# Performance work log

Hardware: AMD Instinct MI355X
Metric: run time of the kernel (lower is better)

Reference implementation:

```python
import jax, jax.numpy as jnp
import numpy as np
import math

B, N, C = 8, 2048, 512

def setup_inputs() -> dict:
    key = jax.random.key(0)
    ks = jax.random.split(key, 7)
    s = 1.0 / math.sqrt(C)
    return {
        "feature": jax.random.normal(ks[0], (B, N, C), dtype=jnp.float32),
        "wq": jax.random.uniform(ks[1], (C, C), jnp.float32, -s, s),
        "bq": jax.random.uniform(ks[2], (C,), jnp.float32, -s, s),
        "wk": jax.random.uniform(ks[3], (C, C), jnp.float32, -s, s),
        "bk": jax.random.uniform(ks[4], (C,), jnp.float32, -s, s),
        "wv": jax.random.uniform(ks[5], (C, C), jnp.float32, -s, s),
        "bv": jax.random.uniform(ks[6], (C,), jnp.float32, -s, s),
    }

def reference(feature, wq, bq, wk, bk, wv, bv):
    # torch nn.Linear: x @ W.T + b
    q = jnp.einsum('bnc,dc->bnd', feature, wq) + bq
    k = jnp.einsum('bnc,dc->bnd', feature, wk) + bk
    v = jnp.einsum('bnc,dc->bnd', feature, wv) + bv
    scores = jnp.einsum('bnd,bmd->bnm', q, k)          # [B, N, N]
    attn = jax.nn.softmax(scores, axis=2) / math.sqrt(C)  # post-softmax scale (as in source)
    v_star = jnp.einsum('bnm,bmd->bnd', attn, v)
    return feature + v_star
```

## Files before the change

### kernel.cpp

```cpp
#include <hip/hip_runtime.h>
#include <cstdint>
#include <cstddef>


typedef __bf16 bf16x8 __attribute__((ext_vector_type(8)));
typedef float f32x4 __attribute__((ext_vector_type(4)));
typedef short short4v __attribute__((ext_vector_type(4)));

__device__ __forceinline__ short f2b(float f) {
  union { float f; unsigned u; } u; u.f = f;
  unsigned r = (u.u + 0x7fffu + ((u.u >> 16) & 1u)) >> 16;
  return (short)r;
}

#define GLDS(gptr, lptr) \
  __builtin_amdgcn_global_load_lds( \
      (const __attribute__((address_space(1))) unsigned int*)(const void*)(gptr), \
      (__attribute__((address_space(3))) unsigned int*)(void*)(lptr), 16, 0, 0)

__device__ __forceinline__ bf16x8 ldfrag64(const short* buf, int row, int kq) {
  return *(const bf16x8*)(buf + row * 64 + ((kq ^ (row & 7)) * 8));
}

__device__ __forceinline__ bf16x8 ldfrag32(const short* buf, int row, int l4) {
  const short* p = buf + row * 32 + ((l4 ^ ((row >> 1) & 3)) * 8);
  bf16x8 r;
  asm volatile("ds_read_b128 %0, %1"
               : "=v"(r)
               : "v"((const __attribute__((address_space(3))) short*)(const void*)p));
  return r;
}

#define LGKM0_SB() do { \
    asm volatile("s_waitcnt lgkmcnt(0)" ::: "memory"); \
    __builtin_amdgcn_sched_barrier(0); } while (0)
#define VMW(n) asm volatile("s_waitcnt vmcnt(" #n ")" ::: "memory")
#define SBAR() __builtin_amdgcn_s_barrier()
#define PRIO1() __builtin_amdgcn_s_setprio(1)
#define PRIO0() __builtin_amdgcn_s_setprio(0)

__global__ __launch_bounds__(256) void prep(const float* __restrict__ f,
                                            const float* __restrict__ w0,
                                            const float* __restrict__ w1,
                                            const float* __restrict__ w2,
                                            const float* __restrict__ b0,
                                            const float* __restrict__ b1,
                                            const float* __restrict__ b2,
                                            short* __restrict__ Xb, short* __restrict__ Wb,
                                            float* __restrict__ biasP, float* __restrict__ l) {
  const int bid = blockIdx.x;
  const int t = threadIdx.x;
  if (bid < 8192) {
    int i = bid * 256 + t;
    float4 v = ((const float4*)f)[i];
    short4v o = { f2b(v.x), f2b(v.y), f2b(v.z), f2b(v.w) };
    *(short4v*)(Xb + (size_t)i * 4) = o;
  } else if (bid < 8960) {
    int i = (bid - 8192) * 256 + t;
    const float* src = (i < 65536) ? w0 : (i < 131072) ? w1 : w2;
    float4 v = ((const float4*)src)[i & 65535];
    short4v o = { f2b(v.x), f2b(v.y), f2b(v.z), f2b(v.w) };
    *(short4v*)(Wb + (size_t)i * 4) = o;
  } else {
    int i = (bid - 8960) * 256 + t;
    float4 z = { 0.f, 0.f, 0.f, 0.f };
    ((float4*)l)[i * 2] = z;
    ((float4*)l)[i * 2 + 1] = z;
    if (i < 1536) {
      const float* s = (i < 512) ? b0 : (i < 1024) ? b1 : b2;
      biasP[i] = s[i & 511];
    }
  }
}

__global__ __launch_bounds__(256) void gemm_qkv(const short* __restrict__ X,
                                                const short* __restrict__ Wall,
                                                const float* __restrict__ biasP,
                                                short* __restrict__ Out,
                                                short* __restrict__ VtOut) {
  __shared__ __align__(16) short Xs[128 * 64];
  __shared__ __align__(16) short Ws[128 * 64];
  const int z = blockIdx.z;
  const short* Wm = Wall + (size_t)z * 262144;
  const int m0 = blockIdx.y * 128, n0 = blockIdx.x * 128;
  const int t = threadIdx.x;
  const int lane = t & 63, w = t >> 6;
  const int wn = (w & 1) * 64, wm = (w >> 1) * 64;
  const int fr = lane & 15, l4 = lane >> 4;

  f32x4 acc[4][4] = {};

  for (int k0 = 0; k0 < 512; k0 += 64) {
    __syncthreads();
#pragma unroll
    for (int u = 0; u < 4; ++u) {
      int cc = t + u * 256;
      int r = cc >> 3, cs = cc & 7;
      int kk = ((cs ^ (r & 7)) * 8);
      GLDS(X + (size_t)(m0 + r) * 512 + k0 + kk, Xs + cc * 8);
      GLDS(Wm + (size_t)(n0 + r) * 512 + k0 + kk, Ws + cc * 8);
    }
    __syncthreads();
#pragma unroll
    for (int h = 0; h < 2; ++h) {
      bf16x8 wf[4], xf[4];
#pragma unroll
      for (int i = 0; i < 4; ++i) wf[i] = ldfrag64(Ws, wn + i * 16 + fr, h * 4 + l4);
#pragma unroll
      for (int j = 0; j < 4; ++j) xf[j] = ldfrag64(Xs, wm + j * 16 + fr, h * 4 + l4);
      if (z < 2) {
#pragma unroll
        for (int i = 0; i < 4; ++i)
#pragma unroll
          for (int j = 0; j < 4; ++j)
            acc[i][j] = __builtin_amdgcn_mfma_f32_16x16x32_bf16(wf[i], xf[j], acc[i][j], 0, 0, 0);
      } else {
#pragma unroll
        for (int i = 0; i < 4; ++i)
#pragma unroll
          for (int j = 0; j < 4; ++j)
            acc[i][j] = __builtin_amdgcn_mfma_f32_16x16x32_bf16(xf[i], wf[j], acc[i][j], 0, 0, 0);
      }
    }
  }

  const int rq = l4 * 4;
  if (z < 2) {
#pragma unroll
    for (int i = 0; i < 4; ++i) {
      int nb = n0 + wn + i * 16 + rq;
      float4 bs = *(const float4*)(biasP + z * 512 + nb);
#pragma unroll
      for (int j = 0; j < 4; ++j) {
        int m = m0 + wm + j * 16 + fr;
        short4v o = { f2b(acc[i][j][0] + bs.x), f2b(acc[i][j][1] + bs.y),
                      f2b(acc[i][j][2] + bs.z), f2b(acc[i][j][3] + bs.w) };
        *(short4v*)(Out + (size_t)z * 8388608 + (size_t)m * 512 + nb) = o;
      }
    }
  } else {
    const int zB = blockIdx.y >> 4;
    const int mb = m0 & 2047;
#pragma unroll
    for (int j = 0; j < 4; ++j) {
      int d = n0 + wn + j * 16 + fr;
      float bd = biasP[1024 + d];
#pragma unroll
      for (int i = 0; i < 4; ++i) {
        int mloc = mb + wm + i * 16 + rq;
        short4v o = { f2b(acc[i][j][0] + bd), f2b(acc[i][j][1] + bd),
                      f2b(acc[i][j][2] + bd), f2b(acc[i][j][3] + bd) };
        *(short4v*)(VtOut + (size_t)zB * 1048576 + (size_t)d * 2048 + mloc) = o;
      }
    }
  }
}

__global__ __launch_bounds__(256) void gemm_qk8(const short* __restrict__ Q,
                                                const short* __restrict__ Kb,
                                                short* __restrict__ P,
                                                float* __restrict__ l) {
  __shared__ __align__(16) short As[2][4096];
  __shared__ __align__(16) short Bs[2][4096];
  const int id = blockIdx.x + blockIdx.y * 16 + blockIdx.z * 256;
  const int swz = (id & 7) * 256 + (id >> 3);
  const int z = swz >> 8;
  const int m0 = (swz & 15) * 128;
  const int n0 = ((swz >> 4) & 15) * 128;
  const short* __restrict__ A = Kb + (size_t)z * 1048576;
  const short* __restrict__ B = Q + (size_t)z * 1048576;
  const int t = threadIdx.x;
  const int lane = t & 63, w = t >> 6;
  const int aw = (w >> 1) * 64, bw = (w & 1) * 64;
  const int fr = lane & 15, l4 = lane >> 4;
  const int r0 = t >> 2, cs = t & 3;
  const int csw = (cs ^ ((r0 >> 1) & 3)) * 8;
  const short* pA = A + (size_t)(m0 + r0) * 512 + csw;
  const short* pB = B + (size_t)(n0 + r0) * 512 + csw;

#define QK_STG(buf, kt) do { \
    GLDS(pA + (kt) * 32, &As[(buf)][t * 8]); \
    GLDS(pA + 64 * 512 + (kt) * 32, &As[(buf)][2048 + t * 8]); \
    GLDS(pB + (kt) * 32, &Bs[(buf)][t * 8]); \
    GLDS(pB + 64 * 512 + (kt) * 32, &Bs[(buf)][2048 + t * 8]); \
  } while (0)

  f32x4 acc[4][4] = {};
  bf16x8 a[4], b[4];

  QK_STG(0, 0); QK_STG(1, 1);

#pragma unroll 1
  for (int kt = 0; kt < 16; ++kt) {
    const int c = kt & 1;
    if (kt >= 1 && kt < 15) QK_STG(c ^ 1, kt + 1);
    if (kt < 15) { VMW(4); } else { VMW(0); }
    SBAR();
#pragma unroll
    for (int i = 0; i < 4; ++i) a[i] = ldfrag32(&As[c][0], aw + i * 16 + fr, l4);
#pragma unroll
    for (int n = 0; n < 4; ++n) b[n] = ldfrag32(&Bs[c][0], bw + n * 16 + fr, l4);
    LGKM0_SB(); PRIO1();
#pragma unroll
    for (int i = 0; i < 4; ++i)
#pragma unroll
      for (int n = 0; n < 4; ++n)
        acc[i][n] = __builtin_amdgcn_mfma_f32_16x16x32_bf16(a[i], b[n], acc[i][n], 0, 0, 0);
    PRIO0(); SBAR();
  }
#undef QK_STG

  const float LOG2E = 1.4426950408889634f;
  float rs[4] = { 0.f, 0.f, 0.f, 0.f };
#pragma unroll
  for (int i = 0; i < 4; ++i) {
    const int key = m0 + aw + i * 16 + l4 * 4;
#pragma unroll
    for (int n = 0; n < 4; ++n) {
      const int q = n0 + bw + n * 16 + fr;
      short4v o;
      float part = 0.f;
#pragma unroll
      for (int r = 0; r < 4; ++r) {
        float e = exp2f(acc[i][n][r] * LOG2E);
        o[r] = f2b(e);
        part += e;
      }
      *(short4v*)(P + (size_t)z * 4194304 + (size_t)q * 2048 + key) = o;
      rs[n] += part;
    }
  }
#pragma unroll
  for (int n = 0; n < 4; ++n) {
    rs[n] += __shfl_xor(rs[n], 16);
    rs[n] += __shfl_xor(rs[n], 32);
  }
  if (l4 == 0) {
#pragma unroll
    for (int n = 0; n < 4; ++n)
      atomicAdd(&l[z * 2048 + n0 + bw + n * 16 + fr], rs[n]);
  }
}

__global__ __launch_bounds__(256) void gemm_pv8(const short* __restrict__ Pm,
                                                const short* __restrict__ Vt,
                                                const float* __restrict__ l,
                                                const float* __restrict__ resid,
                                                float* __restrict__ out, float scale) {
  __shared__ __align__(16) short As[2][4096];
  __shared__ __align__(16) short Bs[2][4096];
  const int id = blockIdx.x + blockIdx.y * 4 + blockIdx.z * 64;
  const int swz = (id & 7) * 64 + (id >> 3);
  const int z = swz >> 6;
  const int d0 = (swz & 3) * 128;
  const int n0 = ((swz >> 2) & 15) * 128;
  const short* __restrict__ A = Vt + (size_t)z * 1048576;
  const short* __restrict__ B = Pm + (size_t)z * 4194304;
  const int t = threadIdx.x;
  const int lane = t & 63, w = t >> 6;
  const int aw = (w >> 1) * 64, bw = (w & 1) * 64;
  const int fr = lane & 15, l4 = lane >> 4;
  const int r0 = t >> 2, cs = t & 3;
  const int csw = (cs ^ ((r0 >> 1) & 3)) * 8;
  const short* pA = A + (size_t)(d0 + r0) * 2048 + csw;
  const short* pB = B + (size_t)(n0 + r0) * 2048 + csw;

#define PV_STG(buf, kt) do { \
    GLDS(pA + (kt) * 32, &As[(buf)][t * 8]); \
    GLDS(pA + (size_t)64 * 2048 + (kt) * 32, &As[(buf)][2048 + t * 8]); \
    GLDS(pB + (kt) * 32, &Bs[(buf)][t * 8]); \
    GLDS(pB + (size_t)64 * 2048 + (kt) * 32, &Bs[(buf)][2048 + t * 8]); \
  } while (0)

  f32x4 acc[4][4] = {};
  bf16x8 a[4], b[4];

  PV_STG(0, 0); PV_STG(1, 1);

#pragma unroll 1
  for (int kt = 0; kt < 64; ++kt) {
    const int c = kt & 1;
    if (kt >= 1 && kt < 63) PV_STG(c ^ 1, kt + 1);
    if (kt < 63) { VMW(4); } else { VMW(0); }
    SBAR();
#pragma unroll
    for (int i = 0; i < 4; ++i) a[i] = ldfrag32(&As[c][0], aw + i * 16 + fr, l4);
#pragma unroll
    for (int n = 0; n < 4; ++n) b[n] = ldfrag32(&Bs[c][0], bw + n * 16 + fr, l4);
    LGKM0_SB(); PRIO1();
#pragma unroll
    for (int i = 0; i < 4; ++i)
#pragma unroll
      for (int n = 0; n < 4; ++n)
        acc[i][n] = __builtin_amdgcn_mfma_f32_16x16x32_bf16(a[i], b[n], acc[i][n], 0, 0, 0);
    PRIO0(); SBAR();
  }
#undef PV_STG

  float linv[4];
#pragma unroll
  for (int n = 0; n < 4; ++n) {
    const int q = n0 + bw + n * 16 + fr;
    linv[n] = scale / l[z * 2048 + q];
  }
#pragma unroll
  for (int n = 0; n < 4; ++n) {
    const int q = n0 + bw + n * 16 + fr;
#pragma unroll
    for (int i = 0; i < 4; ++i) {
      const int d = d0 + aw + i * 16 + l4 * 4;
      const size_t idx = (size_t)z * 1048576 + (size_t)q * 512 + d;
      float4 rv = *(const float4*)(resid + idx);
      float4 o = { rv.x + acc[i][n][0] * linv[n], rv.y + acc[i][n][1] * linv[n],
                   rv.z + acc[i][n][2] * linv[n], rv.w + acc[i][n][3] * linv[n] };
      *(float4*)(out + idx) = o;
    }
  }
}

extern "C" void kernel_launch(void* const* d_in, const int* in_sizes, int n_in,
                              void* d_out, int out_size, void* d_ws, size_t ws_size,
                              hipStream_t stream) {
  const float* feature = (const float*)d_in[0];
  const float* wq = (const float*)d_in[1];
  const float* bq = (const float*)d_in[2];
  const float* wk = (const float*)d_in[3];
  const float* bk = (const float*)d_in[4];
  const float* wv = (const float*)d_in[5];
  const float* bv = (const float*)d_in[6];
  float* out = (float*)d_out;

  const size_t MN = (size_t)16384 * 512;
  short* Xb = (short*)d_ws;
  short* Wb = Xb + MN;
  short* Q = Wb + 786432;
  short* K = Q + MN;
  short* Vt = K + MN;
  short* P = Vt + MN;
  float* biasP = (float*)(P + (size_t)8 * 2048 * 2048);
  float* l = biasP + 1536;

  prep<<<8968, 256, 0, stream>>>(feature, wq, wk, wv, bq, bk, bv, Xb, Wb, biasP, l);

  gemm_qkv<<<dim3(4, 128, 3), 256, 0, stream>>>(Xb, Wb, biasP, Q, Vt);
  gemm_qk8<<<dim3(16, 16, 8), 256, 0, stream>>>(Q, K, P, l);

  const float iscl = 0.044194173824159216f;
  gemm_pv8<<<dim3(4, 16, 8), 256, 0, stream>>>(P, Vt, l, feature, out, iscl);
}
```

Baseline: 238.3 us.

## Restructure QK and PV GEMMs with resident K tile and register-streamed V

The QK kernel now keeps a full 128x512 K tile resident in LDS per block and loops over four 256-query tiles, streaming only Q through double-buffered LDS. This cuts repeated K loads and moves to 512-thread blocks on a 256-block grid. The PV kernel gives each block 64 queries across all 512 output dims. P is streamed through a triple-buffered LDS ring, and V^T fragments are loaded straight from global into registers with one-step prefetch. The larger LDS footprint and register use, plus a grid of only 256 blocks, lower occupancy and may leave CUs underused.

```diff
diff --git a/kernel.cpp b/kernel.cpp
--- a/kernel.cpp
+++ b/kernel.cpp
@@ -22,13 +22,21 @@
   return *(const bf16x8*)(buf + row * 64 + ((kq ^ (row & 7)) * 8));
 }
 
-__device__ __forceinline__ bf16x8 ldfrag32(const short* buf, int row, int l4) {
-  const short* p = buf + row * 32 + ((l4 ^ ((row >> 1) & 3)) * 8);
+__device__ __forceinline__ bf16x8 ds_asm(const short* p) {
   bf16x8 r;
   asm volatile("ds_read_b128 %0, %1"
                : "=v"(r)
                : "v"((const __attribute__((address_space(3))) short*)(const void*)p));
   return r;
+}
+__device__ __forceinline__ bf16x8 ldfragA(const short* buf, int row, int c) {
+  return ds_asm(buf + row * 512 + ((c ^ (row & 7)) * 8));
+}
+__device__ __forceinline__ bf16x8 ldfrag32(const short* buf, int row, int l4) {
+  return ds_asm(buf + row * 32 + ((l4 ^ ((row >> 1) & 3)) * 8));
+}
+__device__ __forceinline__ bf16x8 ldfragP(const short* buf, int row, int c) {
+  return ds_asm(buf + row * 64 + ((c ^ (row & 7)) * 8));
 }
 
 #define LGKM0_SB() do { \
@@ -156,159 +164,193 @@
   }
 }
 
-__global__ __launch_bounds__(256) void gemm_qk8(const short* __restrict__ Q,
+__global__ __launch_bounds__(512) void gemm_qk9(const short* __restrict__ Q,
                                                 const short* __restrict__ Kb,
                                                 short* __restrict__ P,
                                                 float* __restrict__ l) {
-  __shared__ __align__(16) short As[2][4096];
-  __shared__ __align__(16) short Bs[2][4096];
-  const int id = blockIdx.x + blockIdx.y * 16 + blockIdx.z * 256;
-  const int swz = (id & 7) * 256 + (id >> 3);
-  const int z = swz >> 8;
-  const int m0 = (swz & 15) * 128;
-  const int n0 = ((swz >> 4) & 15) * 128;
-  const short* __restrict__ A = Kb + (size_t)z * 1048576;
-  const short* __restrict__ B = Q + (size_t)z * 1048576;
+  __shared__ __align__(16) short As[128 * 512];
+  __shared__ __align__(16) short Bs[2][256 * 32];
+  const int id = blockIdx.x;
+  const int z = id & 7;
+  const int kb = (id >> 3) & 15;
+  const int qh = id >> 7;
+  const int m0 = kb * 128;
+  const short* __restrict__ Ag = Kb + (size_t)z * 1048576 + (size_t)m0 * 512;
+  const short* __restrict__ Bg = Q + (size_t)z * 1048576 + (size_t)(qh * 1024) * 512;
   const int t = threadIdx.x;
   const int lane = t & 63, w = t >> 6;
-  const int aw = (w >> 1) * 64, bw = (w & 1) * 64;
+  const int aw = (w >> 2) * 64, bw = (w & 3) * 64;
   const int fr = lane & 15, l4 = lane >> 4;
-  const int r0 = t >> 2, cs = t & 3;
-  const int csw = (cs ^ ((r0 >> 1) & 3)) * 8;
-  const short* pA = A + (size_t)(m0 + r0) * 512 + csw;
-  const short* pB = B + (size_t)(n0 + r0) * 512 + csw;
-
-#define QK_STG(buf, kt) do { \
-    GLDS(pA + (kt) * 32, &As[(buf)][t * 8]); \
-    GLDS(pA + 64 * 512 + (kt) * 32, &As[(buf)][2048 + t * 8]); \
-    GLDS(pB + (kt) * 32, &Bs[(buf)][t * 8]); \
-    GLDS(pB + 64 * 512 + (kt) * 32, &Bs[(buf)][2048 + t * 8]); \
+  const int br = t >> 2, bc = t & 3;
+  const int bcs1 = (bc ^ ((br >> 1) & 3)) * 8;
+  const int bcs2 = (bc ^ (((br + 128) >> 1) & 3)) * 8;
+
+#define QK_STG_B(buf, qt, kt) do { \
+    GLDS(Bg + (size_t)((qt) * 256 + br) * 512 + (kt) * 32 + bcs1, &Bs[(buf)][t * 8]); \
+    GLDS(Bg + (size_t)((qt) * 256 + br + 128) * 512 + (kt) * 32 + bcs2, \
+         &Bs[(buf)][4096 + t * 8]); \
   } while (0)
 
+#pragma unroll
+  for (int j = 0; j < 16; ++j) {
+    int Lc = t + j * 512;
+    int r = Lc >> 6, c = Lc & 63;
+    GLDS(Ag + (size_t)r * 512 + (c ^ (r & 7)) * 8, As + Lc * 8);
+  }
+  QK_STG_B(0, 0, 0);
+  VMW(0);
+  SBAR();
+
   f32x4 acc[4][4] = {};
-  bf16x8 a[4], b[4];
-
-  QK_STG(0, 0); QK_STG(1, 1);
-
+  const float LOG2E = 1.4426950408889634f;
+
+  for (int qt = 0; qt < 4; ++qt) {
 #pragma unroll 1
-  for (int kt = 0; kt < 16; ++kt) {
-    const int c = kt & 1;
-    if (kt >= 1 && kt < 15) QK_STG(c ^ 1, kt + 1);
-    if (kt < 15) { VMW(4); } else { VMW(0); }
-    SBAR();
-#pragma unroll
-    for (int i = 0; i < 4; ++i) a[i] = ldfrag32(&As[c][0], aw + i * 16 + fr, l4);
-#pragma unroll
-    for (int n = 0; n < 4; ++n) b[n] = ldfrag32(&Bs[c][0], bw + n * 16 + fr, l4);
-    LGKM0_SB(); PRIO1();
-#pragma unroll
-    for (int i = 0; i < 4; ++i)
+    for (int kt = 0; kt < 16; ++kt) {
+      const int p = qt * 16 + kt;
+      const int c = kt & 1;
+      if (p < 63) {
+        const int pn = p + 1;
+        QK_STG_B(c ^ 1, pn >> 4, pn & 15);
+        VMW(2);
+      } else {
+        VMW(0);
+      }
+      SBAR();
+      bf16x8 af[4], bf[4];
+#pragma unroll
+      for (int i = 0; i < 4; ++i) af[i] = ldfragA(As, aw + i * 16 + fr, kt * 4 + l4);
+#pragma unroll
+      for (int n = 0; n < 4; ++n) bf[n] = ldfrag32(&Bs[c][0], bw + n * 16 + fr, l4);
+      LGKM0_SB(); PRIO1();
+#pragma unroll
+      for (int i = 0; i < 4; ++i)
+#pragma unroll
+        for (int n = 0; n < 4; ++n)
+          acc[i][n] = __builtin_amdgcn_mfma_f32_16x16x32_bf16(af[i], bf[n], acc[i][n], 0, 0, 0);
+      PRIO0(); SBAR();
+    }
+    const int qbase = qh * 1024 + qt * 256;
+    float rs[4] = { 0.f, 0.f, 0.f, 0.f };
+#pragma unroll
+    for (int i = 0; i < 4; ++i) {
+      const int key = m0 + aw + i * 16 + l4 * 4;
+#pragma unroll
+      for (int n = 0; n < 4; ++n) {
+        const int q = qbase + bw + n * 16 + fr;
+        short4v o;
+        float part = 0.f;
+#pragma unroll
+        for (int r = 0; r < 4; ++r) {
+          float e = exp2f(acc[i][n][r] * LOG2E);
+          o[r] = f2b(e);
+          part += e;
+        }
+        *(short4v*)(P + (size_t)z * 4194304 + (size_t)q * 2048 + key) = o;
+        rs[n] += part;
+        acc[i][n] = (f32x4){ 0.f, 0.f, 0.f, 0.f };
+      }
+    }
+#pragma unroll
+    for (int n = 0; n < 4; ++n) {
+      rs[n] += __shfl_xor(rs[n], 16);
+      rs[n] += __shfl_xor(rs[n], 32);
+    }
+    if (l4 == 0) {
 #pragma unroll
       for (int n = 0; n < 4; ++n)
-        acc[i][n] = __builtin_amdgcn_mfma_f32_16x16x32_bf16(a[i], b[n], acc[i][n], 0, 0, 0);
-    PRIO0(); SBAR();
-  }
-#undef QK_STG
-
-  const float LOG2E = 1.4426950408889634f;
-  float rs[4] = { 0.f, 0.f, 0.f, 0.f };
-#pragma unroll
-  for (int i = 0; i < 4; ++i) {
-    const int key = m0 + aw + i * 16 + l4 * 4;
-#pragma unroll
-    for (int n = 0; n < 4; ++n) {
-      const int q = n0 + bw + n * 16 + fr;
-      short4v o;
-      float part = 0.f;
-#pragma unroll
-      for (int r = 0; r < 4; ++r) {
-        float e = exp2f(acc[i][n][r] * LOG2E);
-        o[r] = f2b(e);
-        part += e;
-      }
-      *(short4v*)(P + (size_t)z * 4194304 + (size_t)q * 2048 + key) = o;
-      rs[n] += part;
-    }
-  }
-#pragma unroll
-  for (int n = 0; n < 4; ++n) {
-    rs[n] += __shfl_xor(rs[n], 16);
-    rs[n] += __shfl_xor(rs[n], 32);
-  }
-  if (l4 == 0) {
-#pragma unroll
-    for (int n = 0; n < 4; ++n)
-      atomicAdd(&l[z * 2048 + n0 + bw + n * 16 + fr], rs[n]);
-  }
-}
-
-__global__ __launch_bounds__(256) void gemm_pv8(const short* __restrict__ Pm,
+        atomicAdd(&l[z * 2048 + qbase + bw + n * 16 + fr], rs[n]);
+    }
+  }
+#undef QK_STG_B
+}
+
+__global__ __launch_bounds__(512) void gemm_pv9(const short* __restrict__ Pm,
                                                 const short* __restrict__ Vt,
                                                 const float* __restrict__ l,
                                                 const float* __restrict__ resid,
                                                 float* __restrict__ out, float scale) {
-  __shared__ __align__(16) short As[2][4096];
-  __shared__ __align__(16) short Bs[2][4096];
-  const int id = blockIdx.x + blockIdx.y * 4 + blockIdx.z * 64;
-  const int swz = (id & 7) * 64 + (id >> 3);
-  const int z = swz >> 6;
-  const int d0 = (swz & 3) * 128;
-  const int n0 = ((swz >> 2) & 15) * 128;
-  const short* __restrict__ A = Vt + (size_t)z * 1048576;
-  const short* __restrict__ B = Pm + (size_t)z * 4194304;
+  __shared__ __align__(16) short Ps[3][64 * 64];
+  const int id = blockIdx.x;
+  const int z = id & 7;
+  const int q0 = (id >> 3) * 64;
+  const short* __restrict__ Pg = Pm + (size_t)z * 4194304 + (size_t)q0 * 2048;
+  const short* __restrict__ Vg = Vt + (size_t)z * 1048576;
   const int t = threadIdx.x;
   const int lane = t & 63, w = t >> 6;
-  const int aw = (w >> 1) * 64, bw = (w & 1) * 64;
+  const int dw = w * 64;
   const int fr = lane & 15, l4 = lane >> 4;
-  const int r0 = t >> 2, cs = t & 3;
-  const int csw = (cs ^ ((r0 >> 1) & 3)) * 8;
-  const short* pA = A + (size_t)(d0 + r0) * 2048 + csw;
-  const short* pB = B + (size_t)(n0 + r0) * 2048 + csw;
-
-#define PV_STG(buf, kt) do { \
-    GLDS(pA + (kt) * 32, &As[(buf)][t * 8]); \
-    GLDS(pA + (size_t)64 * 2048 + (kt) * 32, &As[(buf)][2048 + t * 8]); \
-    GLDS(pB + (kt) * 32, &Bs[(buf)][t * 8]); \
-    GLDS(pB + (size_t)64 * 2048 + (kt) * 32, &Bs[(buf)][2048 + t * 8]); \
-  } while (0)
+  const int pr = t >> 3, pc = t & 7;
+  const int pcs = (pc ^ (pr & 7)) * 8;
+
+#define PV_STG_P(s, kt) GLDS(Pg + (size_t)pr * 2048 + (kt) * 64 + pcs, &Ps[(s)][t * 8])
+
+  const short* vbase = Vg + (size_t)(dw + fr) * 2048 + l4 * 8;
 
   f32x4 acc[4][4] = {};
-  bf16x8 a[4], b[4];
-
-  PV_STG(0, 0); PV_STG(1, 1);
+  bf16x8 vc[4][2], vn[4][2];
+
+  PV_STG_P(0, 0);
+  PV_STG_P(1, 1);
+#pragma unroll
+  for (int i = 0; i < 4; ++i)
+#pragma unroll
+    for (int kk = 0; kk < 2; ++kk)
+      vc[i][kk] = *(const bf16x8*)(vbase + (size_t)i * 16 * 2048 + kk * 32);
+  VMW(0);
+  SBAR();
 
 #pragma unroll 1
-  for (int kt = 0; kt < 64; ++kt) {
-    const int c = kt & 1;
-    if (kt >= 1 && kt < 63) PV_STG(c ^ 1, kt + 1);
-    if (kt < 63) { VMW(4); } else { VMW(0); }
+  for (int kt = 0; kt < 32; ++kt) {
+    if (kt < 31) {
+#pragma unroll
+      for (int i = 0; i < 4; ++i)
+#pragma unroll
+        for (int kk = 0; kk < 2; ++kk)
+          vn[i][kk] = *(const bf16x8*)(vbase + (size_t)i * 16 * 2048 +
+                                       (size_t)(kt + 1) * 64 + kk * 32);
+    }
+    if (kt < 30) PV_STG_P((kt + 2) % 3, kt + 2);
+    bf16x8 pf[4][2];
+    {
+      const short* Pc = &Ps[kt % 3][0];
+#pragma unroll
+      for (int n = 0; n < 4; ++n)
+#pragma unroll
+        for (int kk = 0; kk < 2; ++kk)
+          pf[n][kk] = ldfragP(Pc, n * 16 + fr, kk * 4 + l4);
+    }
+    if (kt < 30) { VMW(9); } else if (kt == 30) { VMW(8); } else { VMW(0); }
     SBAR();
-#pragma unroll
-    for (int i = 0; i < 4; ++i) a[i] = ldfrag32(&As[c][0], aw + i * 16 + fr, l4);
-#pragma unroll
-    for (int n = 0; n < 4; ++n) b[n] = ldfrag32(&Bs[c][0], bw + n * 16 + fr, l4);
     LGKM0_SB(); PRIO1();
 #pragma unroll
-    for (int i = 0; i < 4; ++i)
-#pragma unroll
-      for (int n = 0; n < 4; ++n)
-        acc[i][n] = __builtin_amdgcn_mfma_f32_16x16x32_bf16(a[i], b[n], acc[i][n], 0, 0, 0);
+    for (int kk = 0; kk < 2; ++kk)
+#pragma unroll
+      for (int i = 0; i < 4; ++i)
+#pragma unroll
+        for (int n = 0; n < 4; ++n)
+          acc[i][n] = __builtin_amdgcn_mfma_f32_16x16x32_bf16(vc[i][kk], pf[n][kk],
+                                                              acc[i][n], 0, 0, 0);
     PRIO0(); SBAR();
-  }
-#undef PV_STG
+    if (kt < 31) {
+#pragma unroll
+      for (int i = 0; i < 4; ++i)
+#pragma unroll
+        for (int kk = 0; kk < 2; ++kk) vc[i][kk] = vn[i][kk];
+    }
+  }
+#undef PV_STG_P
 
   float linv[4];
 #pragma unroll
+  for (int n = 0; n < 4; ++n)
+    linv[n] = scale / l[z * 2048 + q0 + n * 16 + fr];
+#pragma unroll
   for (int n = 0; n < 4; ++n) {
-    const int q = n0 + bw + n * 16 + fr;
-    linv[n] = scale / l[z * 2048 + q];
-  }
-#pragma unroll
-  for (int n = 0; n < 4; ++n) {
-    const int q = n0 + bw + n * 16 + fr;
+    const int q = q0 + n * 16 + fr;
 #pragma unroll
     for (int i = 0; i < 4; ++i) {
-      const int d = d0 + aw + i * 16 + l4 * 4;
+      const int d = dw + i * 16 + l4 * 4;
       const size_t idx = (size_t)z * 1048576 + (size_t)q * 512 + d;
       float4 rv = *(const float4*)(resid + idx);
       float4 o = { rv.x + acc[i][n][0] * linv[n], rv.y + acc[i][n][1] * linv[n],
@@ -343,8 +385,8 @@
   prep<<<8968, 256, 0, stream>>>(feature, wq, wk, wv, bq, bk, bv, Xb, Wb, biasP, l);
 
   gemm_qkv<<<dim3(4, 128, 3), 256, 0, stream>>>(Xb, Wb, biasP, Q, Vt);
-  gemm_qk8<<<dim3(16, 16, 8), 256, 0, stream>>>(Q, K, P, l);
+  gemm_qk9<<<256, 512, 0, stream>>>(Q, K, P, l);
 
   const float iscl = 0.044194173824159216f;
-  gemm_pv8<<<dim3(4, 16, 8), 256, 0, stream>>>(P, Vt, l, feature, out, iscl);
-}
+  gemm_pv9<<<256, 512, 0, stream>>>(P, Vt, l, feature, out, iscl);
+}
```

Result: slower. 287.5 us (+20.7%).

## Enlarge QK and PV GEMM tiles to 1024-thread blocks with K=64 stages

Applied to the files above, without the earlier changes.

Both attention GEMMs move from 128x128 tiles with 256 threads to 1024-thread blocks: QK uses 256x256 tiles and PV uses 128x256 tiles, each with a K step of 64 and an 8-way XOR swizzle. The pipeline changes from prefetching two stages ahead to issuing the next stage's global-to-LDS load after the fragment reads, with a full vmcnt(0) wait per iteration. The larger tiles are meant to cut global and L2 traffic through more reuse, at the cost of far fewer blocks (512 and 256), higher LDS use per block, and a shallower prefetch that may expose memory latency.

```diff
diff --git a/kernel.cpp b/kernel.cpp
--- a/kernel.cpp
+++ b/kernel.cpp
@@ -22,19 +22,21 @@
   return *(const bf16x8*)(buf + row * 64 + ((kq ^ (row & 7)) * 8));
 }
 
-__device__ __forceinline__ bf16x8 ldfrag32(const short* buf, int row, int l4) {
-  const short* p = buf + row * 32 + ((l4 ^ ((row >> 1) & 3)) * 8);
+__device__ __forceinline__ bf16x8 ds_asm(const short* p) {
   bf16x8 r;
   asm volatile("ds_read_b128 %0, %1"
                : "=v"(r)
                : "v"((const __attribute__((address_space(3))) short*)(const void*)p));
   return r;
 }
+__device__ __forceinline__ bf16x8 ldfrag64a(const short* buf, int row, int kq) {
+  return ds_asm(buf + row * 64 + ((kq ^ (row & 7)) * 8));
+}
 
 #define LGKM0_SB() do { \
     asm volatile("s_waitcnt lgkmcnt(0)" ::: "memory"); \
     __builtin_amdgcn_sched_barrier(0); } while (0)
-#define VMW(n) asm volatile("s_waitcnt vmcnt(" #n ")" ::: "memory")
+#define VMW0() asm volatile("s_waitcnt vmcnt(0)" ::: "memory")
 #define SBAR() __builtin_amdgcn_s_barrier()
 #define PRIO1() __builtin_amdgcn_s_setprio(1)
 #define PRIO0() __builtin_amdgcn_s_setprio(0)
@@ -156,57 +158,70 @@
   }
 }
 
-__global__ __launch_bounds__(256) void gemm_qk8(const short* __restrict__ Q,
-                                                const short* __restrict__ Kb,
-                                                short* __restrict__ P,
-                                                float* __restrict__ l) {
-  __shared__ __align__(16) short As[2][4096];
-  __shared__ __align__(16) short Bs[2][4096];
-  const int id = blockIdx.x + blockIdx.y * 16 + blockIdx.z * 256;
-  const int swz = (id & 7) * 256 + (id >> 3);
-  const int z = swz >> 8;
-  const int m0 = (swz & 15) * 128;
-  const int n0 = ((swz >> 4) & 15) * 128;
-  const short* __restrict__ A = Kb + (size_t)z * 1048576;
-  const short* __restrict__ B = Q + (size_t)z * 1048576;
+__global__ __launch_bounds__(1024) void gemm_qk10(const short* __restrict__ Q,
+                                                  const short* __restrict__ Kb,
+                                                  short* __restrict__ P,
+                                                  float* __restrict__ l) {
+  __shared__ __align__(16) short As[2][16384];
+  __shared__ __align__(16) short Bs[2][16384];
+  const int id = blockIdx.x;
+  const int z = id & 7, r = id >> 3;
+  const int m0 = (r & 7) * 256;
+  const int n0 = (r >> 3) * 256;
+  const short* __restrict__ A = Kb + (size_t)z * 1048576 + (size_t)m0 * 512;
+  const short* __restrict__ B = Q + (size_t)z * 1048576 + (size_t)n0 * 512;
   const int t = threadIdx.x;
   const int lane = t & 63, w = t >> 6;
-  const int aw = (w >> 1) * 64, bw = (w & 1) * 64;
+  const int aw = (w >> 2) * 64, bw = (w & 3) * 64;
   const int fr = lane & 15, l4 = lane >> 4;
-  const int r0 = t >> 2, cs = t & 3;
-  const int csw = (cs ^ ((r0 >> 1) & 3)) * 8;
-  const short* pA = A + (size_t)(m0 + r0) * 512 + csw;
-  const short* pB = B + (size_t)(n0 + r0) * 512 + csw;
+  const int sr = t >> 3, sc = t & 7;
+  const int swz = (sc ^ (sr & 7)) * 8;
+  const short* pA = A + (size_t)sr * 512 + swz;
+  const short* pB = B + (size_t)sr * 512 + swz;
 
 #define QK_STG(buf, kt) do { \
-    GLDS(pA + (kt) * 32, &As[(buf)][t * 8]); \
-    GLDS(pA + 64 * 512 + (kt) * 32, &As[(buf)][2048 + t * 8]); \
-    GLDS(pB + (kt) * 32, &Bs[(buf)][t * 8]); \
-    GLDS(pB + 64 * 512 + (kt) * 32, &Bs[(buf)][2048 + t * 8]); \
+    GLDS(pA + (kt) * 64, &As[(buf)][t * 8]); \
+    GLDS(pA + (size_t)128 * 512 + (kt) * 64, &As[(buf)][(t + 1024) * 8]); \
+    GLDS(pB + (kt) * 64, &Bs[(buf)][t * 8]); \
+    GLDS(pB + (size_t)128 * 512 + (kt) * 64, &Bs[(buf)][(t + 1024) * 8]); \
   } while (0)
 
   f32x4 acc[4][4] = {};
   bf16x8 a[4], b[4];
 
-  QK_STG(0, 0); QK_STG(1, 1);
-
-#pragma unroll 1
-  for (int kt = 0; kt < 16; ++kt) {
+  QK_STG(0, 0);
+  VMW0();
+  SBAR();
+
+#pragma unroll 2
+  for (int kt = 0; kt < 8; ++kt) {
     const int c = kt & 1;
-    if (kt >= 1 && kt < 15) QK_STG(c ^ 1, kt + 1);
-    if (kt < 15) { VMW(4); } else { VMW(0); }
+#pragma unroll
+    for (int i = 0; i < 4; ++i) a[i] = ldfrag64a(&As[c][0], aw + i * 16 + fr, l4);
+#pragma unroll
+    for (int n = 0; n < 4; ++n) b[n] = ldfrag64a(&Bs[c][0], bw + n * 16 + fr, l4);
+    if (kt < 7) QK_STG(c ^ 1, kt + 1);
     SBAR();
-#pragma unroll
-    for (int i = 0; i < 4; ++i) a[i] = ldfrag32(&As[c][0], aw + i * 16 + fr, l4);
-#pragma unroll
-    for (int n = 0; n < 4; ++n) b[n] = ldfrag32(&Bs[c][0], bw + n * 16 + fr, l4);
-    LGKM0_SB(); PRIO1();
+    LGKM0_SB();
+    PRIO1();
 #pragma unroll
     for (int i = 0; i < 4; ++i)
 #pragma unroll
       for (int n = 0; n < 4; ++n)
         acc[i][n] = __builtin_amdgcn_mfma_f32_16x16x32_bf16(a[i], b[n], acc[i][n], 0, 0, 0);
-    PRIO0(); SBAR();
+#pragma unroll
+    for (int i = 0; i < 4; ++i) a[i] = ldfrag64a(&As[c][0], aw + i * 16 + fr, 4 + l4);
+#pragma unroll
+    for (int n = 0; n < 4; ++n) b[n] = ldfrag64a(&Bs[c][0], bw + n * 16 + fr, 4 + l4);
+    LGKM0_SB();
+#pragma unroll
+    for (int i = 0; i < 4; ++i)
+#pragma unroll
+      for (int n = 0; n < 4; ++n)
+        acc[i][n] = __builtin_amdgcn_mfma_f32_16x16x32_bf16(a[i], b[n], acc[i][n], 0, 0, 0);
+    PRIO0();
+    if (kt < 7) VMW0();
+    SBAR();
   }
 #undef QK_STG
 
@@ -221,9 +236,9 @@
       short4v o;
       float part = 0.f;
 #pragma unroll
-      for (int r = 0; r < 4; ++r) {
-        float e = exp2f(acc[i][n][r] * LOG2E);
-        o[r] = f2b(e);
+      for (int rr = 0; rr < 4; ++rr) {
+        float e = exp2f(acc[i][n][rr] * LOG2E);
+        o[rr] = f2b(e);
         part += e;
       }
       *(short4v*)(P + (size_t)z * 4194304 + (size_t)q * 2048 + key) = o;
@@ -242,70 +257,80 @@
   }
 }
 
-__global__ __launch_bounds__(256) void gemm_pv8(const short* __restrict__ Pm,
-                                                const short* __restrict__ Vt,
-                                                const float* __restrict__ l,
-                                                const float* __restrict__ resid,
-                                                float* __restrict__ out, float scale) {
-  __shared__ __align__(16) short As[2][4096];
-  __shared__ __align__(16) short Bs[2][4096];
-  const int id = blockIdx.x + blockIdx.y * 4 + blockIdx.z * 64;
-  const int swz = (id & 7) * 64 + (id >> 3);
-  const int z = swz >> 6;
-  const int d0 = (swz & 3) * 128;
-  const int n0 = ((swz >> 2) & 15) * 128;
-  const short* __restrict__ A = Vt + (size_t)z * 1048576;
-  const short* __restrict__ B = Pm + (size_t)z * 4194304;
+__global__ __launch_bounds__(1024) void gemm_pv10(const short* __restrict__ Pm,
+                                                  const short* __restrict__ Vt,
+                                                  const float* __restrict__ l,
+                                                  const float* __restrict__ resid,
+                                                  float* __restrict__ out, float scale) {
+  __shared__ __align__(16) short As[2][8192];
+  __shared__ __align__(16) short Bs[2][16384];
+  const int id = blockIdx.x;
+  const int z = id & 7, r = id >> 3;
+  const int d0 = (r & 3) * 128;
+  const int q0 = (r >> 2) * 256;
+  const short* __restrict__ A = Vt + (size_t)z * 1048576 + (size_t)d0 * 2048;
+  const short* __restrict__ B = Pm + (size_t)z * 4194304 + (size_t)q0 * 2048;
   const int t = threadIdx.x;
   const int lane = t & 63, w = t >> 6;
-  const int aw = (w >> 1) * 64, bw = (w & 1) * 64;
+  const int aw = (w >> 3) * 64, bw = (w & 7) * 32;
   const int fr = lane & 15, l4 = lane >> 4;
-  const int r0 = t >> 2, cs = t & 3;
-  const int csw = (cs ^ ((r0 >> 1) & 3)) * 8;
-  const short* pA = A + (size_t)(d0 + r0) * 2048 + csw;
-  const short* pB = B + (size_t)(n0 + r0) * 2048 + csw;
+  const int sr = t >> 3, sc = t & 7;
+  const int swz = (sc ^ (sr & 7)) * 8;
+  const short* pA = A + (size_t)sr * 2048 + swz;
+  const short* pB = B + (size_t)sr * 2048 + swz;
 
 #define PV_STG(buf, kt) do { \
-    GLDS(pA + (kt) * 32, &As[(buf)][t * 8]); \
-    GLDS(pA + (size_t)64 * 2048 + (kt) * 32, &As[(buf)][2048 + t * 8]); \
-    GLDS(pB + (kt) * 32, &Bs[(buf)][t * 8]); \
-    GLDS(pB + (size_t)64 * 2048 + (kt) * 32, &Bs[(buf)][2048 + t * 8]); \
+    GLDS(pA + (kt) * 64, &As[(buf)][t * 8]); \
+    GLDS(pB + (kt) * 64, &Bs[(buf)][t * 8]); \
+    GLDS(pB + (size_t)128 * 2048 + (kt) * 64, &Bs[(buf)][(t + 1024) * 8]); \
   } while (0)
 
-  f32x4 acc[4][4] = {};
-  bf16x8 a[4], b[4];
-
-  PV_STG(0, 0); PV_STG(1, 1);
-
-#pragma unroll 1
-  for (int kt = 0; kt < 64; ++kt) {
+  f32x4 acc[4][2] = {};
+  bf16x8 a[4], b[2];
+
+  PV_STG(0, 0);
+  VMW0();
+  SBAR();
+
+#pragma unroll 2
+  for (int kt = 0; kt < 32; ++kt) {
     const int c = kt & 1;
-    if (kt >= 1 && kt < 63) PV_STG(c ^ 1, kt + 1);
-    if (kt < 63) { VMW(4); } else { VMW(0); }
+#pragma unroll
+    for (int i = 0; i < 4; ++i) a[i] = ldfrag64a(&As[c][0], aw + i * 16 + fr, l4);
+#pragma unroll
+    for (int n = 0; n < 2; ++n) b[n] = ldfrag64a(&Bs[c][0], bw + n * 16 + fr, l4);
+    if (kt < 31) PV_STG(c ^ 1, kt + 1);
     SBAR();
-#pragma unroll
-    for (int i = 0; i < 4; ++i) a[i] = ldfrag32(&As[c][0], aw + i * 16 + fr, l4);
-#pragma unroll
-    for (int n = 0; n < 4; ++n) b[n] = ldfrag32(&Bs[c][0], bw + n * 16 + fr, l4);
-    LGKM0_SB(); PRIO1();
+    LGKM0_SB();
+    PRIO1();
 #pragma unroll
     for (int i = 0; i < 4; ++i)
 #pragma unroll
-      for (int n = 0; n < 4; ++n)
+      for (int n = 0; n < 2; ++n)
         acc[i][n] = __builtin_amdgcn_mfma_f32_16x16x32_bf16(a[i], b[n], acc[i][n], 0, 0, 0);
-    PRIO0(); SBAR();
+#pragma unroll
+    for (int i = 0; i < 4; ++i) a[i] = ldfrag64a(&As[c][0], aw + i * 16 + fr, 4 + l4);
+#pragma unroll
+    for (int n = 0; n < 2; ++n) b[n] = ldfrag64a(&Bs[c][0], bw + n * 16 + fr, 4 + l4);
+    LGKM0_SB();
+#pragma unroll
+    for (int i = 0; i < 4; ++i)
+#pragma unroll
+      for (int n = 0; n < 2; ++n)
+        acc[i][n] = __builtin_amdgcn_mfma_f32_16x16x32_bf16(a[i], b[n], acc[i][n], 0, 0, 0);
+    PRIO0();
+    if (kt < 31) VMW0();
+    SBAR();
   }
 #undef PV_STG
 
-  float linv[4];
-#pragma unroll
-  for (int n = 0; n < 4; ++n) {
-    const int q = n0 + bw + n * 16 + fr;
-    linv[n] = scale / l[z * 2048 + q];
-  }
-#pragma unroll
-  for (int n = 0; n < 4; ++n) {
-    const int q = n0 + bw + n * 16 + fr;
+  float linv[2];
+#pragma unroll
+  for (int n = 0; n < 2; ++n)
+    linv[n] = scale / l[z * 2048 + q0 + bw + n * 16 + fr];
+#pragma unroll
+  for (int n = 0; n < 2; ++n) {
+    const int q = q0 + bw + n * 16 + fr;
 #pragma unroll
     for (int i = 0; i < 4; ++i) {
       const int d = d0 + aw + i * 16 + l4 * 4;
@@ -343,8 +368,8 @@
   prep<<<8968, 256, 0, stream>>>(feature, wq, wk, wv, bq, bk, bv, Xb, Wb, biasP, l);
 
   gemm_qkv<<<dim3(4, 128, 3), 256, 0, stream>>>(Xb, Wb, biasP, Q, Vt);
-  gemm_qk8<<<dim3(16, 16, 8), 256, 0, stream>>>(Q, K, P, l);
+  gemm_qk10<<<512, 1024, 0, stream>>>(Q, K, P, l);
 
   const float iscl = 0.044194173824159216f;
-  gemm_pv8<<<dim3(4, 16, 8), 256, 0, stream>>>(P, Vt, l, feature, out, iscl);
-}
+  gemm_pv10<<<256, 1024, 0, stream>>>(P, Vt, l, feature, out, iscl);
+}
```

New measurement: 276.5 us. +16.0%, slower.
